# Optimization experiments

Hardware: AMD Instinct MI355X
Metric: run time of the kernel (lower is better)

## Reference

```python
import jax, jax.numpy as jnp
import numpy as np


def setup_inputs() -> dict:
    key = jax.random.key(0)
    x = jax.random.normal(key, (16, 64, 256, 256), dtype=jnp.float32)
    return {"x": x}


def reference(x):
    # x: [B, C, H, W]
    b, c, h, w = x.shape
    # L2 norm over channel dim -> [B, 1, H, W]
    weights = jnp.sqrt(jnp.sum(x * x, axis=1, keepdims=True))
    # softmax over height (dim=2)
    weights = jax.nn.softmax(weights, axis=2)
    # weighted sum over height -> [B, C, 1, W]
    weighted_sum = jnp.sum(x * weights, axis=2, keepdims=True)
    weight_sum = jnp.sum(weights, axis=2, keepdims=True)  # [B, 1, 1, W]
    compressed = weighted_sum / (weight_sum + 1e-8)
    # broadcast-repeat along height -> [B, C, H, W]
    out = jnp.broadcast_to(compressed, (b, c, h, w))
    return out
```

## Files before the change

kernel.cpp:

```cpp
#include <hip/hip_runtime.h>


constexpr int B = 16, C = 64, H = 256, W = 256, W4 = 64;
constexpr int HC = 32;
constexpr int HPC = H / HC;
constexpr float KSUB = 8.0f;

typedef float nfloat4 __attribute__((ext_vector_type(4)));

__device__ __forceinline__ float4 f4add(float4 a, float4 b) {
    return make_float4(a.x + b.x, a.y + b.y, a.z + b.z, a.w + b.w);
}

__global__ __launch_bounds__(512) void k_pass1(const float* __restrict__ x,
                                               float4* __restrict__ pcomp,
                                               float4* __restrict__ pden) {
    int blk = blockIdx.x;
    int b = blk >> 5, hc = blk & 31;
    int t = threadIdx.x;
    int lane = t & 63, wave = t >> 6;
    int c8 = lane >> 3;
    int w8 = lane & 7;
    int w4 = wave * 8 + w8;
    int h0 = hc * HPC;

    const float4* xb = (const float4*)x + ((size_t)(b * C + c8) * H + h0) * W4 + w4;
    constexpr size_t CSTRIDE = (size_t)8 * H * W4;

    float4 acc[8];
#pragma unroll
    for (int j = 0; j < 8; ++j) acc[j] = make_float4(0.f, 0.f, 0.f, 0.f);
    float4 dacc = make_float4(0.f, 0.f, 0.f, 0.f);

#pragma unroll
    for (int hh = 0; hh < HPC; ++hh) {
        float4 xv[8];
#pragma unroll
        for (int j = 0; j < 8; ++j)
            xv[j] = xb[(size_t)j * CSTRIDE + (size_t)hh * W4];
        float4 ps = make_float4(0.f, 0.f, 0.f, 0.f);
#pragma unroll
        for (int j = 0; j < 8; ++j) {
            ps.x += xv[j].x * xv[j].x; ps.y += xv[j].y * xv[j].y;
            ps.z += xv[j].z * xv[j].z; ps.w += xv[j].w * xv[j].w;
        }
#pragma unroll
        for (int m = 8; m <= 32; m <<= 1) {
            ps.x += __shfl_xor(ps.x, m);
            ps.y += __shfl_xor(ps.y, m);
            ps.z += __shfl_xor(ps.z, m);
            ps.w += __shfl_xor(ps.w, m);
        }
        float4 e = make_float4(__expf(sqrtf(ps.x) - KSUB), __expf(sqrtf(ps.y) - KSUB),
                               __expf(sqrtf(ps.z) - KSUB), __expf(sqrtf(ps.w) - KSUB));
        dacc = f4add(dacc, e);
#pragma unroll
        for (int j = 0; j < 8; ++j) {
            acc[j].x += xv[j].x * e.x; acc[j].y += xv[j].y * e.y;
            acc[j].z += xv[j].z * e.z; acc[j].w += xv[j].w * e.w;
        }
    }

    size_t pc = ((size_t)(b * HC + hc) * C + c8) * W4 + w4;
#pragma unroll
    for (int j = 0; j < 8; ++j)
        pcomp[pc + (size_t)(8 * j) * W4] = acc[j];
    if (c8 == 0)
        pden[(size_t)(b * HC + hc) * W4 + w4] = dacc;
}

__global__ __launch_bounds__(256) void k_pass2(const float4* __restrict__ pcomp,
                                               const float4* __restrict__ pden,
                                               float* __restrict__ out) {
    __shared__ float4 redc[4][64], redd[4][64];
    int blk = blockIdx.x;
    int b = blk >> 6, c = blk & 63;
    int t = threadIdx.x, hq = t >> 6, w4 = t & 63;

    float4 sc = make_float4(0.f, 0.f, 0.f, 0.f), sd = sc;
#pragma unroll
    for (int k = 0; k < 8; ++k) {
        int hc = hq * 8 + k;
        sc = f4add(sc, pcomp[((size_t)(b * HC + hc) * C + c) * W4 + w4]);
        sd = f4add(sd, pden[(size_t)(b * HC + hc) * W4 + w4]);
    }
    redc[hq][w4] = sc;
    redd[hq][w4] = sd;
    __syncthreads();
    float4 Cs = f4add(f4add(redc[0][w4], redc[1][w4]), f4add(redc[2][w4], redc[3][w4]));
    float4 Ds = f4add(f4add(redd[0][w4], redd[1][w4]), f4add(redd[2][w4], redd[3][w4]));
    nfloat4 f = { Cs.x / (Ds.x * (1.0f + 1e-8f)),
                  Cs.y / (Ds.y * (1.0f + 1e-8f)),
                  Cs.z / (Ds.z * (1.0f + 1e-8f)),
                  Cs.w / (Ds.w * (1.0f + 1e-8f)) };
    nfloat4* op = (nfloat4*)out + (size_t)(b * C + c) * H * W4;
    for (int i = t; i < H * W4; i += 256)
        __builtin_nontemporal_store(f, op + i);
}

extern "C" void kernel_launch(void* const* d_in, const int* in_sizes, int n_in,
                              void* d_out, int out_size, void* d_ws, size_t ws_size,
                              hipStream_t stream) {
    const float* x = (const float*)d_in[0];
    float* out = (float*)d_out;
    float4* pcomp = (float4*)d_ws;
    float4* pden  = pcomp + (size_t)B * HC * C * W4;

    k_pass1<<<B * HC, 512, 0, stream>>>(x, pcomp, pden);
    k_pass2<<<B * C,  256, 0, stream>>>(pcomp, pden, out);
}
```

Baseline: 463.7 us.

## Fuse the two passes into one kernel with per-block W-slices and LDS reduction

Replaces the two-kernel scheme (per-height-chunk partials in workspace, then a second reduce-and-broadcast kernel) with one kernel. Each block owns one batch and a 16-column W slice and loops over all 256 rows. The H reduction happens in registers, through a wave shuffle and through LDS, and the same block writes the broadcast output. This removes the workspace round trip and one launch. In exchange the grid drops to 256 blocks, global accesses become 64-byte contiguous chunks per 4 lanes, and the nontemporal store hint is dropped.

Result: slower. 489.6 us (+5.6%).

```diff
diff --git a/kernel.cpp b/kernel.cpp
--- a/kernel.cpp
+++ b/kernel.cpp
@@ -2,42 +2,42 @@
 
 
 constexpr int B = 16, C = 64, H = 256, W = 256, W4 = 64;
-constexpr int HC = 32;
-constexpr int HPC = H / HC;
 constexpr float KSUB = 8.0f;
-
-typedef float nfloat4 __attribute__((ext_vector_type(4)));
 
 __device__ __forceinline__ float4 f4add(float4 a, float4 b) {
     return make_float4(a.x + b.x, a.y + b.y, a.z + b.z, a.w + b.w);
 }
 
-__global__ __launch_bounds__(512) void k_pass1(const float* __restrict__ x,
-                                               float4* __restrict__ pcomp,
-                                               float4* __restrict__ pden) {
+__global__ __launch_bounds__(512, 4) void k_fused(const float* __restrict__ x,
+                                                  float4* __restrict__ out4) {
+    __shared__ float4 part[8][64][4];
+    __shared__ float4 denp[8][4];
+    __shared__ float4 fin[64][4];
+
     int blk = blockIdx.x;
-    int b = blk >> 5, hc = blk & 31;
+    int m = blk >> 7, g = blk & 127;
+    int b = g >> 3, wo = ((g & 7) << 1) | m;
     int t = threadIdx.x;
-    int lane = t & 63, wave = t >> 6;
-    int c8 = lane >> 3;
-    int w8 = lane & 7;
-    int w4 = wave * 8 + w8;
-    int h0 = hc * HPC;
+    int wave = t >> 6, lane = t & 63;
+    int hbit = lane >> 5;
+    int c8   = (lane >> 2) & 7;
+    int w2   = lane & 3;
+    int w4   = wo * 4 + w2;
 
-    const float4* xb = (const float4*)x + ((size_t)(b * C + c8) * H + h0) * W4 + w4;
-    constexpr size_t CSTRIDE = (size_t)8 * H * W4;
+    const float4* xb = (const float4*)x + ((size_t)(b * C + c8) * H) * W4 + w4;
+    constexpr size_t CSTR = (size_t)8 * H * W4;
 
     float4 acc[8];
 #pragma unroll
     for (int j = 0; j < 8; ++j) acc[j] = make_float4(0.f, 0.f, 0.f, 0.f);
     float4 dacc = make_float4(0.f, 0.f, 0.f, 0.f);
 
-#pragma unroll
-    for (int hh = 0; hh < HPC; ++hh) {
+    for (int k = 0; k < 16; ++k) {
+        int h = wave * 2 + hbit + 16 * k;
         float4 xv[8];
 #pragma unroll
         for (int j = 0; j < 8; ++j)
-            xv[j] = xb[(size_t)j * CSTRIDE + (size_t)hh * W4];
+            xv[j] = xb[(size_t)j * CSTR + (size_t)h * W4];
         float4 ps = make_float4(0.f, 0.f, 0.f, 0.f);
 #pragma unroll
         for (int j = 0; j < 8; ++j) {
@@ -45,11 +45,11 @@
             ps.z += xv[j].z * xv[j].z; ps.w += xv[j].w * xv[j].w;
         }
 #pragma unroll
-        for (int m = 8; m <= 32; m <<= 1) {
-            ps.x += __shfl_xor(ps.x, m);
-            ps.y += __shfl_xor(ps.y, m);
-            ps.z += __shfl_xor(ps.z, m);
-            ps.w += __shfl_xor(ps.w, m);
+        for (int msk = 4; msk <= 16; msk <<= 1) {
+            ps.x += __shfl_xor(ps.x, msk);
+            ps.y += __shfl_xor(ps.y, msk);
+            ps.z += __shfl_xor(ps.z, msk);
+            ps.w += __shfl_xor(ps.w, msk);
         }
         float4 e = make_float4(__expf(sqrtf(ps.x) - KSUB), __expf(sqrtf(ps.y) - KSUB),
                                __expf(sqrtf(ps.z) - KSUB), __expf(sqrtf(ps.w) - KSUB));
@@ -61,51 +61,53 @@
         }
     }
 
-    size_t pc = ((size_t)(b * HC + hc) * C + c8) * W4 + w4;
 #pragma unroll
-    for (int j = 0; j < 8; ++j)
-        pcomp[pc + (size_t)(8 * j) * W4] = acc[j];
-    if (c8 == 0)
-        pden[(size_t)(b * HC + hc) * W4 + w4] = dacc;
-}
+    for (int j = 0; j < 8; ++j) {
+        acc[j].x += __shfl_xor(acc[j].x, 32); acc[j].y += __shfl_xor(acc[j].y, 32);
+        acc[j].z += __shfl_xor(acc[j].z, 32); acc[j].w += __shfl_xor(acc[j].w, 32);
+    }
+    dacc.x += __shfl_xor(dacc.x, 32); dacc.y += __shfl_xor(dacc.y, 32);
+    dacc.z += __shfl_xor(dacc.z, 32); dacc.w += __shfl_xor(dacc.w, 32);
 
-__global__ __launch_bounds__(256) void k_pass2(const float4* __restrict__ pcomp,
-                                               const float4* __restrict__ pden,
-                                               float* __restrict__ out) {
-    __shared__ float4 redc[4][64], redd[4][64];
-    int blk = blockIdx.x;
-    int b = blk >> 6, c = blk & 63;
-    int t = threadIdx.x, hq = t >> 6, w4 = t & 63;
+    if (hbit == 0) {
+#pragma unroll
+        for (int j = 0; j < 8; ++j)
+            part[wave][c8 + 8 * j][w2] = acc[j];
+        if (c8 == 0) denp[wave][w2] = dacc;
+    }
+    __syncthreads();
 
-    float4 sc = make_float4(0.f, 0.f, 0.f, 0.f), sd = sc;
+    if (t < 256) {
+        int c = t >> 2, wq = t & 3;
+        float4 Cs = make_float4(0.f, 0.f, 0.f, 0.f), Ds = Cs;
 #pragma unroll
-    for (int k = 0; k < 8; ++k) {
-        int hc = hq * 8 + k;
-        sc = f4add(sc, pcomp[((size_t)(b * HC + hc) * C + c) * W4 + w4]);
-        sd = f4add(sd, pden[(size_t)(b * HC + hc) * W4 + w4]);
+        for (int wv = 0; wv < 8; ++wv) {
+            Cs = f4add(Cs, part[wv][c][wq]);
+            Ds = f4add(Ds, denp[wv][wq]);
+        }
+        fin[c][wq] = make_float4(Cs.x / (Ds.x * (1.0f + 1e-8f)),
+                                 Cs.y / (Ds.y * (1.0f + 1e-8f)),
+                                 Cs.z / (Ds.z * (1.0f + 1e-8f)),
+                                 Cs.w / (Ds.w * (1.0f + 1e-8f)));
     }
-    redc[hq][w4] = sc;
-    redd[hq][w4] = sd;
     __syncthreads();
-    float4 Cs = f4add(f4add(redc[0][w4], redc[1][w4]), f4add(redc[2][w4], redc[3][w4]));
-    float4 Ds = f4add(f4add(redd[0][w4], redd[1][w4]), f4add(redd[2][w4], redd[3][w4]));
-    nfloat4 f = { Cs.x / (Ds.x * (1.0f + 1e-8f)),
-                  Cs.y / (Ds.y * (1.0f + 1e-8f)),
-                  Cs.z / (Ds.z * (1.0f + 1e-8f)),
-                  Cs.w / (Ds.w * (1.0f + 1e-8f)) };
-    nfloat4* op = (nfloat4*)out + (size_t)(b * C + c) * H * W4;
-    for (int i = t; i < H * W4; i += 256)
-        __builtin_nontemporal_store(f, op + i);
+
+    int h128 = t >> 2, wq = t & 3;
+    float4* ob = out4 + (size_t)b * C * H * W4 + (size_t)wo * 4 + wq;
+    for (int c = 0; c < C; ++c) {
+        float4 f = fin[c][wq];
+        size_t base = (size_t)c * H * W4;
+        ob[base + (size_t)h128 * W4]         = f;
+        ob[base + (size_t)(h128 + 128) * W4] = f;
+    }
 }
 
 extern "C" void kernel_launch(void* const* d_in, const int* in_sizes, int n_in,
                               void* d_out, int out_size, void* d_ws, size_t ws_size,
                               hipStream_t stream) {
     const float* x = (const float*)d_in[0];
-    float* out = (float*)d_out;
-    float4* pcomp = (float4*)d_ws;
-    float4* pden  = pcomp + (size_t)B * HC * C * W4;
+    float4* out4 = (float4*)d_out;
+    (void)d_ws; (void)ws_size;
 
-    k_pass1<<<B * HC, 512, 0, stream>>>(x, pcomp, pden);
-    k_pass2<<<B * C,  256, 0, stream>>>(pcomp, pden, out);
+    k_fused<<<B * 16, 512, 0, stream>>>(x, out4);
 }
```
